# Kernel tuning notes

Hardware: AMD Instinct MI355X
Metric: run time of the kernel (lower is better)

Reference implementation:

```python
import jax, jax.numpy as jnp
from jax import lax
import numpy as np

B = 262144      # batch (scaled from toy 10)
T = 5           # timesteps, hard-coded in source reshape [_, 5, 1]
D_IN = 1        # input feature dim
UNITS = 64      # LSTM units (scaled from toy 10)


def setup_inputs() -> dict:
    key = jax.random.key(0)
    ks = jax.random.split(key, 5)
    x = jax.random.normal(ks[0], (B, T, D_IN), dtype=jnp.float32)
    # Keras LSTM params: kernel [D_IN, 4*units], recurrent_kernel [units, 4*units], bias [4*units]
    W = jax.random.normal(ks[1], (D_IN, 4 * UNITS), dtype=jnp.float32) * 0.5
    U = jax.random.normal(ks[2], (UNITS, 4 * UNITS), dtype=jnp.float32) * (1.0 / np.sqrt(UNITS))
    b = jnp.zeros((4 * UNITS,), dtype=jnp.float32)
    Wd = jax.random.normal(ks[3], (UNITS, 1), dtype=jnp.float32) * (1.0 / np.sqrt(UNITS))
    bd = jnp.zeros((1,), dtype=jnp.float32)
    return {"x": x, "W": W, "U": U, "b": b, "Wd": Wd, "bd": bd}


def reference(x, W, U, b, Wd, bd):
    # Faithful to: x = reshape(input, [B, T, 1]); x = LSTM(units)(x); out = Dense(1, relu)(x)
    units = U.shape[0]
    batch = x.shape[0]
    xs = jnp.transpose(x, (1, 0, 2))  # [T, B, D_IN] for scan over time

    def step(carry, xt):
        h, c = carry
        z = xt @ W + h @ U + b            # [B, 4*units]
        i, f, g, o = jnp.split(z, 4, axis=-1)  # Keras gate order: i, f, c~, o
        i = jax.nn.sigmoid(i)
        f = jax.nn.sigmoid(f)
        g = jnp.tanh(g)
        o = jax.nn.sigmoid(o)
        c = f * c + i * g
        h = o * jnp.tanh(c)
        return (h, c), None

    h0 = jnp.zeros((batch, units), dtype=x.dtype)
    (h_last, _), _ = lax.scan(step, (h0, h0), xs)
    # Dense(1, activation='relu')
    return jax.nn.relu(h_last @ Wd + bd)  # [B, 1]
```

## Files before the change

kernel.cpp:

```cpp
#include <hip/hip_runtime.h>


typedef _Float16 f16x8 __attribute__((ext_vector_type(8)));
typedef float f32x4 __attribute__((ext_vector_type(4)));
typedef float f32x2 __attribute__((ext_vector_type(2)));

#define MB 64
#define NTHREADS 256
#define HSTR 68

__device__ __forceinline__ float ex2(float x) { return __builtin_amdgcn_exp2f(x); }
__device__ __forceinline__ float rcp(float x) { return __builtin_amdgcn_rcpf(x); }
__device__ __forceinline__ f32x2 fma2(f32x2 a, f32x2 b, f32x2 c) {
    return __builtin_elementwise_fma(a, b, c);
}

__global__ __launch_bounds__(NTHREADS, 3) void lstm_fused(
    const float* __restrict__ x,
    const float* __restrict__ W,
    const float* __restrict__ U,
    const float* __restrict__ b,
    const float* __restrict__ Wd,
    const float* __restrict__ bd,
    float* __restrict__ out,
    int B)
{
    __shared__ _Float16 hbuf[2][64 * HSTR];
    __shared__ float xs[5][MB];
    __shared__ float red[4][64];
    __shared__ float wds[64];

    const int tid  = threadIdx.x;
    const int wv   = tid >> 6;
    const int lane = tid & 63;
    const int l15  = lane & 15;
    const int quad = lane >> 4;
    const int row0 = blockIdx.x * MB;

    for (int i = tid; i < MB * 5; i += NTHREADS)
        xs[i % 5][i / 5] = x[row0 * 5 + i];
    if (tid < 64) wds[tid] = Wd[tid];

    const float LOG2E = 1.44269504f;
    const float gscale[4] = {-LOG2E, -LOG2E, -2.0f * LOG2E, -LOG2E};
    const float CSC = -2.0f * LOG2E;

    const int ncol = wv * 16 + l15;
    float Wf[4], bf[4];
    f16x8 Bf[4][2];
#pragma unroll
    for (int g = 0; g < 4; ++g) {
        const int n = g * 64 + ncol;
        const float s = gscale[g];
        Wf[g] = W[n] * s;
        bf[g] = b[n] * s;
#pragma unroll
        for (int kh = 0; kh < 2; ++kh) {
            f16x8 v;
#pragma unroll
            for (int j = 0; j < 8; ++j) {
                const int k = kh * 32 + quad * 8 + j;
                v[j] = (_Float16)(U[k * 256 + n] * s);
            }
            Bf[g][kh] = v;
            asm volatile("" : "+v"(Bf[g][kh]));
        }
    }

    f32x2 cst[4][2];
#pragma unroll
    for (int a = 0; a < 4; ++a)
#pragma unroll
        for (int pr = 0; pr < 2; ++pr) cst[a][pr] = (f32x2){0.f, 0.f};

    __syncthreads();

#pragma unroll
    for (int rt = 0; rt < 4; ++rt) {
        const f32x4 xv = *(const f32x4*)&xs[0][rt * 16 + quad * 4];
#pragma unroll
        for (int pr = 0; pr < 2; ++pr) {
            const f32x2 xp = {xv[2 * pr], xv[2 * pr + 1]};
            const f32x2 zi = fma2(xp, (f32x2){Wf[0], Wf[0]}, (f32x2){bf[0], bf[0]});
            const f32x2 zg = fma2(xp, (f32x2){Wf[2], Wf[2]}, (f32x2){bf[2], bf[2]});
            const f32x2 zo = fma2(xp, (f32x2){Wf[3], Wf[3]}, (f32x2){bf[3], bf[3]});
            const f32x2 ei = {ex2(zi.x), ex2(zi.y)};
            const f32x2 eg = {ex2(zg.x), ex2(zg.y)};
            const f32x2 eo = {ex2(zo.x), ex2(zo.y)};
            const f32x2 pq = (1.0f + ei) * (1.0f + eg);
            const f32x2 r1 = {rcp(pq.x), rcp(pq.y)};
            const f32x2 cn = (1.0f - eg) * r1;
            cst[rt][pr] = cn;
            const f32x2 sc = cn * CSC;
            const f32x2 ec = {ex2(sc.x), ex2(sc.y)};
            const f32x2 dn = (1.0f + eo) * (1.0f + ec);
            const f32x2 r2 = {rcp(dn.x), rcp(dn.y)};
            const f32x2 h2 = (1.0f - ec) * r2;
            const int rb = rt * 16 + quad * 4 + 2 * pr;
            hbuf[0][rb * HSTR + ncol]       = (_Float16)h2.x;
            hbuf[0][(rb + 1) * HSTR + ncol] = (_Float16)h2.y;
        }
    }

#pragma unroll
    for (int t = 1; t < 5; ++t) {
        const int src = (t + 1) & 1;
        const int dst = t & 1;
        __syncthreads();
#pragma unroll
        for (int rt = 0; rt < 4; ++rt) {
            const int arow = rt * 16 + l15;
            const f16x8 a0 = *(const f16x8*)&hbuf[src][arow * HSTR + quad * 8];
            const f16x8 a1 = *(const f16x8*)&hbuf[src][arow * HSTR + 32 + quad * 8];
            const f32x4 xv = *(const f32x4*)&xs[t][rt * 16 + quad * 4];
            const f32x2 xlo = {xv[0], xv[1]};
            const f32x2 xhi = {xv[2], xv[3]};
            f32x4 acc[4];
#pragma unroll
            for (int g = 0; g < 4; ++g) {
                const f32x2 wg = {Wf[g], Wf[g]};
                const f32x2 bg = {bf[g], bf[g]};
                const f32x2 zlo = fma2(xlo, wg, bg);
                const f32x2 zhi = fma2(xhi, wg, bg);
                f32x4 z = {zlo.x, zlo.y, zhi.x, zhi.y};
                z = __builtin_amdgcn_mfma_f32_16x16x32_f16(a0, Bf[g][0], z, 0, 0, 0);
                z = __builtin_amdgcn_mfma_f32_16x16x32_f16(a1, Bf[g][1], z, 0, 0, 0);
                acc[g] = z;
            }
#pragma unroll
            for (int pr = 0; pr < 2; ++pr) {
                const f32x2 ei = {ex2(acc[0][2 * pr]), ex2(acc[0][2 * pr + 1])};
                const f32x2 ef = {ex2(acc[1][2 * pr]), ex2(acc[1][2 * pr + 1])};
                const f32x2 eg = {ex2(acc[2][2 * pr]), ex2(acc[2][2 * pr + 1])};
                const f32x2 eo = {ex2(acc[3][2 * pr]), ex2(acc[3][2 * pr + 1])};
                const f32x2 p  = (1.0f + ei) * (1.0f + eg);
                const f32x2 q  = 1.0f + ef;
                const f32x2 num = fma2(cst[rt][pr], p, q * (1.0f - eg));
                const f32x2 pq  = p * q;
                const f32x2 ipq = {rcp(pq.x), rcp(pq.y)};
                const f32x2 cn  = num * ipq;
                cst[rt][pr] = cn;
                const f32x2 sc = cn * CSC;
                const f32x2 ec = {ex2(sc.x), ex2(sc.y)};
                const f32x2 dn = (1.0f + eo) * (1.0f + ec);
                const f32x2 r2 = {rcp(dn.x), rcp(dn.y)};
                const f32x2 h2 = (1.0f - ec) * r2;
                const int rb = rt * 16 + quad * 4 + 2 * pr;
                hbuf[dst][rb * HSTR + ncol]       = (_Float16)h2.x;
                hbuf[dst][(rb + 1) * HSTR + ncol] = (_Float16)h2.y;
            }
        }
    }

    __syncthreads();

    {
        const int row = tid & 63;
        const int q   = tid >> 6;
        float s = 0.0f;
#pragma unroll
        for (int j = 0; j < 16; ++j)
            s += (float)hbuf[0][row * HSTR + q * 16 + j] * wds[q * 16 + j];
        red[q][row] = s;
    }
    __syncthreads();
    if (tid < 64) {
        const float r = red[0][tid] + red[1][tid] + red[2][tid] + red[3][tid] + bd[0];
        out[row0 + tid] = fmaxf(r, 0.0f);
    }
}

extern "C" void kernel_launch(void* const* d_in, const int* in_sizes, int n_in,
                              void* d_out, int out_size, void* d_ws, size_t ws_size,
                              hipStream_t stream) {
    const float* x  = (const float*)d_in[0];
    const float* W  = (const float*)d_in[1];
    const float* U  = (const float*)d_in[2];
    const float* b  = (const float*)d_in[3];
    const float* Wd = (const float*)d_in[4];
    const float* bd = (const float*)d_in[5];
    float* out = (float*)d_out;
    const int B = in_sizes[0] / 5;
    const int grid = B / MB;
    lstm_fused<<<grid, NTHREADS, 0, stream>>>(x, W, U, b, Wd, bd, out, B);
}
```

Baseline: 141.6 us.

## Give each wave its own 16-row batch tile to drop block barriers

Restructures work so each of 8 waves owns 16 batch rows and computes all 256 gate columns, rather than 4 waves splitting columns over 64 shared rows. The hidden state stays in a per-wave LDS slice, which removes the per-timestep __syncthreads and the cross-wave reduction in the dense head (now done with lane shuffles). The U fragments move from registers into shared LDS, and W and b are packed into LDS too, with each block building them once. This trades block-wide barriers for extra LDS reads of B fragments on every MFMA, and it relies on wave-local ordering of LDS writes and reads enforced only by compiler memory fences.

Result: slower. 148.6 us (+4.9%).

```diff
diff --git a/kernel.cpp b/kernel.cpp
--- a/kernel.cpp
+++ b/kernel.cpp
@@ -5,8 +5,9 @@
 typedef float f32x4 __attribute__((ext_vector_type(4)));
 typedef float f32x2 __attribute__((ext_vector_type(2)));
 
-#define MB 64
-#define NTHREADS 256
+#define NTHREADS 512
+#define WPB 8
+#define MB (WPB * 16)
 #define HSTR 68
 
 __device__ __forceinline__ float ex2(float x) { return __builtin_amdgcn_exp2f(x); }
@@ -15,7 +16,7 @@
     return __builtin_elementwise_fma(a, b, c);
 }
 
-__global__ __launch_bounds__(NTHREADS, 3) void lstm_fused(
+__global__ __launch_bounds__(NTHREADS, 4) void lstm_fused(
     const float* __restrict__ x,
     const float* __restrict__ W,
     const float* __restrict__ U,
@@ -25,9 +26,10 @@
     float* __restrict__ out,
     int B)
 {
-    __shared__ _Float16 hbuf[2][64 * HSTR];
+    __shared__ f16x8 bfrag[16][2][64];
+    __shared__ _Float16 hb[WPB][16 * HSTR];
     __shared__ float xs[5][MB];
-    __shared__ float red[4][64];
+    __shared__ f32x2 wb[256];
     __shared__ float wds[64];
 
     const int tid  = threadIdx.x;
@@ -37,35 +39,34 @@
     const int quad = lane >> 4;
     const int row0 = blockIdx.x * MB;
 
+    const float LOG2E = 1.44269504f;
+    const float CSC = -2.0f * LOG2E;
+
     for (int i = tid; i < MB * 5; i += NTHREADS)
         xs[i % 5][i / 5] = x[row0 * 5 + i];
     if (tid < 64) wds[tid] = Wd[tid];
+    if (tid < 256) {
+        const int g = tid >> 6;
+        const float s = (g == 2) ? -2.0f * LOG2E : -LOG2E;
+        wb[tid] = (f32x2){W[tid] * s, b[tid] * s};
+    }
+    for (int e = tid; e < 16 * 2 * 64; e += NTHREADS) {
+        const int le = e & 63;
+        const int kh = (e >> 6) & 1;
+        const int nt = e >> 7;
+        const int g  = nt >> 2;
+        const int n  = g * 64 + (nt & 3) * 16 + (le & 15);
+        const int qe = le >> 4;
+        const float s = (g == 2) ? -2.0f * LOG2E : -LOG2E;
+        f16x8 v;
+#pragma unroll
+        for (int j = 0; j < 8; ++j)
+            v[j] = (_Float16)(U[(kh * 32 + qe * 8 + j) * 256 + n] * s);
+        bfrag[nt][kh][le] = v;
+    }
+    __syncthreads();
 
-    const float LOG2E = 1.44269504f;
-    const float gscale[4] = {-LOG2E, -LOG2E, -2.0f * LOG2E, -LOG2E};
-    const float CSC = -2.0f * LOG2E;
-
-    const int ncol = wv * 16 + l15;
-    float Wf[4], bf[4];
-    f16x8 Bf[4][2];
-#pragma unroll
-    for (int g = 0; g < 4; ++g) {
-        const int n = g * 64 + ncol;
-        const float s = gscale[g];
-        Wf[g] = W[n] * s;
-        bf[g] = b[n] * s;
-#pragma unroll
-        for (int kh = 0; kh < 2; ++kh) {
-            f16x8 v;
-#pragma unroll
-            for (int j = 0; j < 8; ++j) {
-                const int k = kh * 32 + quad * 8 + j;
-                v[j] = (_Float16)(U[k * 256 + n] * s);
-            }
-            Bf[g][kh] = v;
-            asm volatile("" : "+v"(Bf[g][kh]));
-        }
-    }
+    _Float16* const hw = &hb[wv][0];
 
     f32x2 cst[4][2];
 #pragma unroll
@@ -73,58 +74,61 @@
 #pragma unroll
         for (int pr = 0; pr < 2; ++pr) cst[a][pr] = (f32x2){0.f, 0.f};
 
-    __syncthreads();
-
+    {
+        const f32x4 xv = *(const f32x4*)&xs[0][wv * 16 + quad * 4];
 #pragma unroll
-    for (int rt = 0; rt < 4; ++rt) {
-        const f32x4 xv = *(const f32x4*)&xs[0][rt * 16 + quad * 4];
+        for (int sub = 0; sub < 4; ++sub) {
+            const f32x2 wbi = wb[0 * 64 + sub * 16 + l15];
+            const f32x2 wbg = wb[2 * 64 + sub * 16 + l15];
+            const f32x2 wbo = wb[3 * 64 + sub * 16 + l15];
 #pragma unroll
-        for (int pr = 0; pr < 2; ++pr) {
-            const f32x2 xp = {xv[2 * pr], xv[2 * pr + 1]};
-            const f32x2 zi = fma2(xp, (f32x2){Wf[0], Wf[0]}, (f32x2){bf[0], bf[0]});
-            const f32x2 zg = fma2(xp, (f32x2){Wf[2], Wf[2]}, (f32x2){bf[2], bf[2]});
-            const f32x2 zo = fma2(xp, (f32x2){Wf[3], Wf[3]}, (f32x2){bf[3], bf[3]});
-            const f32x2 ei = {ex2(zi.x), ex2(zi.y)};
-            const f32x2 eg = {ex2(zg.x), ex2(zg.y)};
-            const f32x2 eo = {ex2(zo.x), ex2(zo.y)};
-            const f32x2 pq = (1.0f + ei) * (1.0f + eg);
-            const f32x2 r1 = {rcp(pq.x), rcp(pq.y)};
-            const f32x2 cn = (1.0f - eg) * r1;
-            cst[rt][pr] = cn;
-            const f32x2 sc = cn * CSC;
-            const f32x2 ec = {ex2(sc.x), ex2(sc.y)};
-            const f32x2 dn = (1.0f + eo) * (1.0f + ec);
-            const f32x2 r2 = {rcp(dn.x), rcp(dn.y)};
-            const f32x2 h2 = (1.0f - ec) * r2;
-            const int rb = rt * 16 + quad * 4 + 2 * pr;
-            hbuf[0][rb * HSTR + ncol]       = (_Float16)h2.x;
-            hbuf[0][(rb + 1) * HSTR + ncol] = (_Float16)h2.y;
+            for (int pr = 0; pr < 2; ++pr) {
+                const f32x2 xp = {xv[2 * pr], xv[2 * pr + 1]};
+                const f32x2 ei = {ex2(__builtin_fmaf(xp.x, wbi.x, wbi.y)),
+                                  ex2(__builtin_fmaf(xp.y, wbi.x, wbi.y))};
+                const f32x2 eg = {ex2(__builtin_fmaf(xp.x, wbg.x, wbg.y)),
+                                  ex2(__builtin_fmaf(xp.y, wbg.x, wbg.y))};
+                const f32x2 eo = {ex2(__builtin_fmaf(xp.x, wbo.x, wbo.y)),
+                                  ex2(__builtin_fmaf(xp.y, wbo.x, wbo.y))};
+                const f32x2 pq = (1.0f + ei) * (1.0f + eg);
+                const f32x2 r1 = {rcp(pq.x), rcp(pq.y)};
+                const f32x2 cn = (1.0f - eg) * r1;
+                cst[sub][pr] = cn;
+                const f32x2 sc = cn * CSC;
+                const f32x2 ec = {ex2(sc.x), ex2(sc.y)};
+                const f32x2 dn = (1.0f + eo) * (1.0f + ec);
+                const f32x2 r2 = {rcp(dn.x), rcp(dn.y)};
+                const f32x2 h2 = (1.0f - ec) * r2;
+                const int row = quad * 4 + 2 * pr;
+                const int col = sub * 16 + l15;
+                hw[row * HSTR + col]       = (_Float16)h2.x;
+                hw[(row + 1) * HSTR + col] = (_Float16)h2.y;
+            }
         }
     }
 
 #pragma unroll
     for (int t = 1; t < 5; ++t) {
-        const int src = (t + 1) & 1;
-        const int dst = t & 1;
-        __syncthreads();
+        asm volatile("" ::: "memory");
+        const f16x8 a0 = *(const f16x8*)&hw[l15 * HSTR + quad * 8];
+        const f16x8 a1 = *(const f16x8*)&hw[l15 * HSTR + 32 + quad * 8];
+        asm volatile("" ::: "memory");
+        const f32x4 xv = *(const f32x4*)&xs[t][wv * 16 + quad * 4];
+        const f32x2 xlo = {xv[0], xv[1]};
+        const f32x2 xhi = {xv[2], xv[3]};
 #pragma unroll
-        for (int rt = 0; rt < 4; ++rt) {
-            const int arow = rt * 16 + l15;
-            const f16x8 a0 = *(const f16x8*)&hbuf[src][arow * HSTR + quad * 8];
-            const f16x8 a1 = *(const f16x8*)&hbuf[src][arow * HSTR + 32 + quad * 8];
-            const f32x4 xv = *(const f32x4*)&xs[t][rt * 16 + quad * 4];
-            const f32x2 xlo = {xv[0], xv[1]};
-            const f32x2 xhi = {xv[2], xv[3]};
+        for (int sub = 0; sub < 4; ++sub) {
             f32x4 acc[4];
 #pragma unroll
             for (int g = 0; g < 4; ++g) {
-                const f32x2 wg = {Wf[g], Wf[g]};
-                const f32x2 bg = {bf[g], bf[g]};
+                const f32x2 wv2 = wb[g * 64 + sub * 16 + l15];
+                const f32x2 wg = {wv2.x, wv2.x};
+                const f32x2 bg = {wv2.y, wv2.y};
                 const f32x2 zlo = fma2(xlo, wg, bg);
                 const f32x2 zhi = fma2(xhi, wg, bg);
                 f32x4 z = {zlo.x, zlo.y, zhi.x, zhi.y};
-                z = __builtin_amdgcn_mfma_f32_16x16x32_f16(a0, Bf[g][0], z, 0, 0, 0);
-                z = __builtin_amdgcn_mfma_f32_16x16x32_f16(a1, Bf[g][1], z, 0, 0, 0);
+                z = __builtin_amdgcn_mfma_f32_16x16x32_f16(a0, bfrag[g * 4 + sub][0][lane], z, 0, 0, 0);
+                z = __builtin_amdgcn_mfma_f32_16x16x32_f16(a1, bfrag[g * 4 + sub][1][lane], z, 0, 0, 0);
                 acc[g] = z;
             }
 #pragma unroll
@@ -135,38 +139,44 @@
                 const f32x2 eo = {ex2(acc[3][2 * pr]), ex2(acc[3][2 * pr + 1])};
                 const f32x2 p  = (1.0f + ei) * (1.0f + eg);
                 const f32x2 q  = 1.0f + ef;
-                const f32x2 num = fma2(cst[rt][pr], p, q * (1.0f - eg));
+                const f32x2 num = fma2(cst[sub][pr], p, q * (1.0f - eg));
                 const f32x2 pq  = p * q;
                 const f32x2 ipq = {rcp(pq.x), rcp(pq.y)};
                 const f32x2 cn  = num * ipq;
-                cst[rt][pr] = cn;
+                cst[sub][pr] = cn;
                 const f32x2 sc = cn * CSC;
                 const f32x2 ec = {ex2(sc.x), ex2(sc.y)};
                 const f32x2 dn = (1.0f + eo) * (1.0f + ec);
                 const f32x2 r2 = {rcp(dn.x), rcp(dn.y)};
                 const f32x2 h2 = (1.0f - ec) * r2;
-                const int rb = rt * 16 + quad * 4 + 2 * pr;
-                hbuf[dst][rb * HSTR + ncol]       = (_Float16)h2.x;
-                hbuf[dst][(rb + 1) * HSTR + ncol] = (_Float16)h2.y;
+                const int row = quad * 4 + 2 * pr;
+                const int col = sub * 16 + l15;
+                hw[row * HSTR + col]       = (_Float16)h2.x;
+                hw[(row + 1) * HSTR + col] = (_Float16)h2.y;
             }
         }
     }
 
-    __syncthreads();
-
+    asm volatile("" ::: "memory");
     {
-        const int row = tid & 63;
-        const int q   = tid >> 6;
+        const f16x8 hv0 = *(const f16x8*)&hw[l15 * HSTR + quad * 16];
+        const f16x8 hv1 = *(const f16x8*)&hw[l15 * HSTR + quad * 16 + 8];
+        const f32x4 w0 = *(const f32x4*)&wds[quad * 16];
+        const f32x4 w1 = *(const f32x4*)&wds[quad * 16 + 4];
+        const f32x4 w2 = *(const f32x4*)&wds[quad * 16 + 8];
+        const f32x4 w3 = *(const f32x4*)&wds[quad * 16 + 12];
         float s = 0.0f;
 #pragma unroll
-        for (int j = 0; j < 16; ++j)
-            s += (float)hbuf[0][row * HSTR + q * 16 + j] * wds[q * 16 + j];
-        red[q][row] = s;
-    }
-    __syncthreads();
-    if (tid < 64) {
-        const float r = red[0][tid] + red[1][tid] + red[2][tid] + red[3][tid] + bd[0];
-        out[row0 + tid] = fmaxf(r, 0.0f);
+        for (int j = 0; j < 4; ++j) {
+            s = __builtin_fmaf((float)hv0[j],     w0[j], s);
+            s = __builtin_fmaf((float)hv0[4 + j], w1[j], s);
+            s = __builtin_fmaf((float)hv1[j],     w2[j], s);
+            s = __builtin_fmaf((float)hv1[4 + j], w3[j], s);
+        }
+        s += __shfl_xor(s, 16);
+        s += __shfl_xor(s, 32);
+        if (quad == 0)
+            out[row0 + wv * 16 + l15] = fmaxf(s + bd[0], 0.0f);
     }
 }
 
```
